# Kernel tuning notes

Measured on AMD Instinct MI355X. Metric: run time of the kernel, lower is better.

The kernel has to match this reference:

```python
import jax, jax.numpy as jnp
import numpy as np

N = 100000      # nodes
E = 1600000     # edges
D_IN = 100
D_OUT = 100


def _sage(x, src, dst, W_agg, W_root, b):
    """PyG SAGEConv, aggr='mean', root_weight=True:
    out = mean_{j in N(i)} x_j @ W_agg + x_i @ W_root + b
    Aggregation flows source -> target (dst gathers from src)."""
    num_nodes = x.shape[0]
    deg = jax.ops.segment_sum(jnp.ones((src.shape[0],), x.dtype), dst,
                              num_segments=num_nodes)
    agg = jax.ops.segment_sum(x[src], dst, num_segments=num_nodes)  # [N, D]
    agg = agg / jnp.maximum(deg, 1.0)[:, None]
    return agg @ W_agg + x @ W_root + b


def setup_inputs() -> dict:
    key = jax.random.key(0)
    ks = jax.random.split(key, 12)
    s = 0.05
    return {
        "x": jax.random.normal(ks[0], (N, D_IN), jnp.float32),
        "edge_index": jax.random.randint(ks[1], (2, E), 0, N, jnp.int32),
        "edge_weight": jax.random.uniform(ks[2], (E,), jnp.float32),
        "W_sage_agg": jax.random.normal(ks[3], (D_IN, D_OUT), jnp.float32) * s,
        "W_sage_root": jax.random.normal(ks[4], (D_IN, D_OUT), jnp.float32) * s,
        "b_sage": jnp.zeros((D_OUT,), jnp.float32),
        "W_mu_agg": jax.random.normal(ks[5], (D_OUT, D_OUT), jnp.float32) * s,
        "W_mu_root": jax.random.normal(ks[6], (D_OUT, D_OUT), jnp.float32) * s,
        "b_mu": jnp.zeros((D_OUT,), jnp.float32),
        "W_var_agg": jax.random.normal(ks[7], (D_OUT, D_OUT), jnp.float32) * s,
        "W_var_root": jax.random.normal(ks[8], (D_OUT, D_OUT), jnp.float32) * s,
        "b_var": jnp.zeros((D_OUT,), jnp.float32),
    }


def reference(x, edge_index, edge_weight,
              W_sage_agg, W_sage_root, b_sage,
              W_mu_agg, W_mu_root, b_mu,
              W_var_agg, W_var_root, b_var):
    # edge_weight is accepted but unused, matching the torch module.
    src, dst = edge_index[0], edge_index[1]
    feat = jax.nn.relu(_sage(x, src, dst, W_sage_agg, W_sage_root, b_sage))
    mu = _sage(feat, src, dst, W_mu_agg, W_mu_root, b_mu)
    var = _sage(feat, src, dst, W_var_agg, W_var_root, b_var)
    return (mu, var)
```

## Files before the change

### kernel.cpp

```cpp
#include <hip/hip_runtime.h>
#include <cstdint>
#include <cstddef>

#define N_NODES 100000
#define N_EDGES 1600000
#define DIM 100
#define DPAD 128
#define ROWS_ALLOC 100096

#define RPB 128
#define GEMM_GRID (ROWS_ALLOC / RPB)

#define KBUCK 500
#define NPB   200
#define BCAP  4096
#define EPB   6400

typedef __attribute__((ext_vector_type(8))) short s16x8;
typedef __attribute__((ext_vector_type(8))) unsigned short us8;
typedef __attribute__((ext_vector_type(4))) unsigned short us4;
typedef __attribute__((ext_vector_type(4))) float f32x4;
typedef __attribute__((ext_vector_type(2))) float f32x2;
typedef __attribute__((ext_vector_type(4))) unsigned int u32x4;

static __device__ __forceinline__ float bf2f(unsigned short h) {
    return __uint_as_float(((unsigned)h) << 16);
}
static __device__ __forceinline__ unsigned short f2bf(float f) {
    unsigned u = __float_as_uint(f);
    return (unsigned short)((u + 0x7FFFu + ((u >> 16) & 1u)) >> 16);
}

__global__ __launch_bounds__(256) void bucket_kernel(const int* __restrict__ ei,
                                                     unsigned* __restrict__ bucket_cur,
                                                     unsigned* __restrict__ regions) {
    __shared__ unsigned hist[KBUCK];
    __shared__ unsigned posl[KBUCK];
    int tid = threadIdx.x;
    int e0 = blockIdx.x * EPB;
    for (int i = tid; i < KBUCK; i += 256) hist[i] = 0;
    __syncthreads();
    for (int i = tid; i < EPB; i += 256) {
        int dst = ei[N_EDGES + e0 + i];
        int b = dst / NPB;
        atomicAdd(&hist[b], 1u);
    }
    __syncthreads();
    for (int i = tid; i < KBUCK; i += 256) {
        unsigned h = hist[i];
        posl[i] = h ? atomicAdd(&bucket_cur[i], h) : 0u;
    }
    __syncthreads();
    for (int i = tid; i < EPB; i += 256) {
        int src = ei[e0 + i];
        int dst = ei[N_EDGES + e0 + i];
        int b = dst / NPB;
        int dl = dst - b * NPB;
        unsigned r = atomicAdd(&posl[b], 1u);
        if (r < BCAP) regions[(size_t)b * BCAP + r] = ((unsigned)src << 8) | (unsigned)dl;
    }
}

__global__ __launch_bounds__(256) void csr_kernel(const unsigned* __restrict__ regions,
                                                  const unsigned* __restrict__ bucket_cur,
                                                  unsigned* __restrict__ gbase,
                                                  int* __restrict__ row_off,
                                                  int* __restrict__ cnt,
                                                  int* __restrict__ csr_src) {
    __shared__ unsigned hist[256];
    __shared__ unsigned sa[256], sb[256];
    __shared__ unsigned posl[256];
    __shared__ unsigned sh_gb;
    int tid = threadIdx.x;
    int b = blockIdx.x;
    unsigned total = bucket_cur[b];
    if (total > BCAP) total = BCAP;
    hist[tid] = 0;
    __syncthreads();
    const unsigned* reg = regions + (size_t)b * BCAP;
    for (unsigned e = tid; e < total; e += 256)
        atomicAdd(&hist[reg[e] & 0xFFu], 1u);
    __syncthreads();
    unsigned* cur = sa; unsigned* nxt = sb;
    cur[tid] = hist[tid];
    __syncthreads();
    for (int off = 1; off < 256; off <<= 1) {
        unsigned t = cur[tid];
        if (tid >= off) t += cur[tid - off];
        nxt[tid] = t;
        __syncthreads();
        unsigned* tmp = cur; cur = nxt; nxt = tmp;
    }
    unsigned excl = cur[tid] - hist[tid];
    if (tid == 0) sh_gb = atomicAdd(gbase, total);
    __syncthreads();
    unsigned gb = sh_gb;
    posl[tid] = gb + excl;
    if (tid < NPB) {
        int node = b * NPB + tid;
        cnt[node] = (int)hist[tid];
        row_off[node] = (int)(gb + excl);
    }
    __syncthreads();
    for (unsigned e = tid; e < total; e += 256) {
        unsigned p = reg[e];
        unsigned r = atomicAdd(&posl[p & 0xFFu], 1u);
        csr_src[r] = (int)(p >> 8);
    }
}

__global__ __launch_bounds__(256) void convert_pad(const float* __restrict__ X,
                                                   unsigned short* __restrict__ Xp) {
    int t = blockIdx.x * 256 + threadIdx.x;
    if (t >= N_NODES * 16) return;
    int node = t >> 4, chunk = t & 15;
    us8 o;
    if (chunk < 12) {
        const float4* p = (const float4*)(X + (size_t)node * DIM + chunk * 8);
        float4 a = p[0], b = p[1];
        o[0] = f2bf(a.x); o[1] = f2bf(a.y); o[2] = f2bf(a.z); o[3] = f2bf(a.w);
        o[4] = f2bf(b.x); o[5] = f2bf(b.y); o[6] = f2bf(b.z); o[7] = f2bf(b.w);
    } else if (chunk == 12) {
        const float4* p = (const float4*)(X + (size_t)node * DIM + 96);
        float4 a = p[0];
        o[0] = f2bf(a.x); o[1] = f2bf(a.y); o[2] = f2bf(a.z); o[3] = f2bf(a.w);
        o[4] = 0; o[5] = 0; o[6] = 0; o[7] = 0;
    } else {
        for (int i = 0; i < 8; ++i) o[i] = 0;
    }
    *(us8*)(Xp + (size_t)node * DPAD + chunk * 8) = o;
}

__global__ __launch_bounds__(256) void build_w(const float* __restrict__ W0, const float* __restrict__ W1,
                                               const float* __restrict__ W2, const float* __restrict__ W3,
                                               const float* __restrict__ W4, const float* __restrict__ W5,
                                               unsigned short* __restrict__ Wt) {
    int t = blockIdx.x * 256 + threadIdx.x;
    if (t >= 6 * DPAD * 16) return;
    int mat = t / (DPAD * 16);
    int rem = t % (DPAD * 16);
    int nrow = rem >> 4, chunk = rem & 15;
    const float* W = (mat == 0) ? W0 : (mat == 1) ? W1 : (mat == 2) ? W2
                   : (mat == 3) ? W3 : (mat == 4) ? W4 : W5;
    us8 o;
    #pragma unroll
    for (int j = 0; j < 8; ++j) {
        int k = chunk * 8 + j;
        float v = (k < DIM && nrow < DIM) ? W[(size_t)k * DIM + nrow] : 0.f;
        o[j] = f2bf(v);
    }
    *(us8*)(Wt + (size_t)mat * DPAD * DPAD + (size_t)nrow * DPAD + chunk * 8) = o;
}

__global__ __launch_bounds__(256) void build_bias(const float* __restrict__ b0, const float* __restrict__ b1,
                                                  const float* __restrict__ b2, float* __restrict__ bp) {
    int t = blockIdx.x * 256 + threadIdx.x;
    if (t >= 3 * DPAD) return;
    int mat = t / DPAD, i = t % DPAD;
    const float* b = (mat == 0) ? b0 : (mat == 1) ? b1 : b2;
    bp[t] = (i < DIM) ? b[i] : 0.f;
}

__global__ __launch_bounds__(256) void aggregate_pad(const unsigned short* __restrict__ Xh,
                                                     const int* __restrict__ csr_src,
                                                     const int* __restrict__ row_off,
                                                     const int* __restrict__ cnt,
                                                     unsigned short* __restrict__ outh, int n) {
    int node = blockIdx.x * 4 + (threadIdx.x >> 6);
    if (node >= n) return;
    int lane  = threadIdx.x & 63;
    int chunk = lane & 15;
    int slot  = lane >> 4;
    int start = row_off[node];
    int deg   = cnt[node];

    f32x2 acc2[4];
    #pragma unroll
    for (int k = 0; k < 4; ++k) acc2[k] = (f32x2){0.f, 0.f};

    const int coff = chunk * 8;
    int base = 0;
    for (; base + 16 <= deg; base += 16) {
        const int* ep = csr_src + start + base + slot * 4;
        int s0 = ep[0], s1 = ep[1], s2 = ep[2], s3 = ep[3];
        u32x4 w0 = *(const u32x4*)(Xh + (size_t)s0 * DPAD + coff);
        u32x4 w1 = *(const u32x4*)(Xh + (size_t)s1 * DPAD + coff);
        u32x4 w2 = *(const u32x4*)(Xh + (size_t)s2 * DPAD + coff);
        u32x4 w3 = *(const u32x4*)(Xh + (size_t)s3 * DPAD + coff);
        #pragma unroll
        for (int k = 0; k < 4; ++k) {
            acc2[k] += (f32x2){__uint_as_float(w0[k] << 16), __uint_as_float(w0[k] & 0xFFFF0000u)};
            acc2[k] += (f32x2){__uint_as_float(w1[k] << 16), __uint_as_float(w1[k] & 0xFFFF0000u)};
            acc2[k] += (f32x2){__uint_as_float(w2[k] << 16), __uint_as_float(w2[k] & 0xFFFF0000u)};
            acc2[k] += (f32x2){__uint_as_float(w3[k] << 16), __uint_as_float(w3[k] & 0xFFFF0000u)};
        }
    }
    if (base < deg) {
        int e0 = base + slot * 4;
        #pragma unroll
        for (int t = 0; t < 4; ++t) {
            int el = e0 + t;
            bool ok = el < deg;
            int eg = start + (ok ? el : (deg - 1));
            int s  = csr_src[eg];
            u32x4 w = *(const u32x4*)(Xh + (size_t)s * DPAD + coff);
            float mval = ok ? 1.f : 0.f;
            f32x2 mm = (f32x2){mval, mval};
            #pragma unroll
            for (int k = 0; k < 4; ++k) {
                f32x2 v = (f32x2){__uint_as_float(w[k] << 16), __uint_as_float(w[k] & 0xFFFF0000u)};
                acc2[k] += v * mm;
            }
        }
    }
    #pragma unroll
    for (int k = 0; k < 4; ++k) {
        acc2[k].x += __shfl_xor(acc2[k].x, 16, 64);
        acc2[k].y += __shfl_xor(acc2[k].y, 16, 64);
        acc2[k].x += __shfl_xor(acc2[k].x, 32, 64);
        acc2[k].y += __shfl_xor(acc2[k].y, 32, 64);
    }
    if (lane < 16) {
        float inv = 1.0f / (float)(deg > 0 ? deg : 1);
        us8 o;
        #pragma unroll
        for (int k = 0; k < 4; ++k) {
            o[2 * k]     = f2bf(acc2[k].x * inv);
            o[2 * k + 1] = f2bf(acc2[k].y * inv);
        }
        *(us8*)(outh + (size_t)node * DPAD + coff) = o;
    }
}

__global__ __launch_bounds__(256, 2) void gemm_l1_strip(const unsigned short* __restrict__ Aagg,
                                                        const unsigned short* __restrict__ Aroot,
                                                        const unsigned short* __restrict__ WtA,
                                                        const unsigned short* __restrict__ WtR,
                                                        const float* __restrict__ bpad,
                                                        unsigned short* __restrict__ outp) {
    int lane  = threadIdx.x & 63;
    int strip = threadIdx.x >> 6;
    int m16   = lane & 15;
    int quad  = lane >> 4;
    int row0  = blockIdx.x * RPB;

    s16x8 wf[2][2][4];
    const unsigned short* Ws[2] = {WtA, WtR};
    #pragma unroll
    for (int ph = 0; ph < 2; ++ph)
        #pragma unroll
        for (int nt = 0; nt < 2; ++nt)
            #pragma unroll
            for (int ks = 0; ks < 4; ++ks)
                wf[ph][nt][ks] = *(const s16x8*)(Ws[ph] + (size_t)(strip * 32 + nt * 16 + m16) * DPAD + ks * 32 + quad * 8);
    #pragma unroll
    for (int ph = 0; ph < 2; ++ph)
        #pragma unroll
        for (int nt = 0; nt < 2; ++nt)
            #pragma unroll
            for (int ks = 0; ks < 4; ++ks)
                asm volatile("" : "+v"(wf[ph][nt][ks]));

    float4 bias4[2];
    #pragma unroll
    for (int nt = 0; nt < 2; ++nt)
        bias4[nt] = *(const float4*)(bpad + strip * 32 + nt * 16 + quad * 4);

    s16x8 bA[2][4], bR[2][4];
    #pragma unroll
    for (int ks = 0; ks < 4; ++ks) {
        bA[0][ks] = *(const s16x8*)(Aagg  + (size_t)(row0 + m16) * DPAD + ks * 32 + quad * 8);
        bR[0][ks] = *(const s16x8*)(Aroot + (size_t)(row0 + m16) * DPAD + ks * 32 + quad * 8);
    }

    #pragma unroll
    for (int t = 0; t < RPB / 16; ++t) {
        int cur = t & 1;
        if (t < RPB / 16 - 1) {
            int mn = row0 + (t + 1) * 16 + m16;
            #pragma unroll
            for (int ks = 0; ks < 4; ++ks) {
                bA[cur ^ 1][ks] = *(const s16x8*)(Aagg  + (size_t)mn * DPAD + ks * 32 + quad * 8);
                bR[cur ^ 1][ks] = *(const s16x8*)(Aroot + (size_t)mn * DPAD + ks * 32 + quad * 8);
            }
        }
        f32x4 acc[2];
        acc[0] = (f32x4){0.f, 0.f, 0.f, 0.f};
        acc[1] = (f32x4){0.f, 0.f, 0.f, 0.f};
        #pragma unroll
        for (int ks = 0; ks < 4; ++ks) {
            acc[0] = __builtin_amdgcn_mfma_f32_16x16x32_bf16(wf[0][0][ks], bA[cur][ks], acc[0], 0, 0, 0);
            acc[1] = __builtin_amdgcn_mfma_f32_16x16x32_bf16(wf[0][1][ks], bA[cur][ks], acc[1], 0, 0, 0);
            acc[0] = __builtin_amdgcn_mfma_f32_16x16x32_bf16(wf[1][0][ks], bR[cur][ks], acc[0], 0, 0, 0);
            acc[1] = __builtin_amdgcn_mfma_f32_16x16x32_bf16(wf[1][1][ks], bR[cur][ks], acc[1], 0, 0, 0);
        }
        int m = row0 + t * 16 + m16;
        #pragma unroll
        for (int nt = 0; nt < 2; ++nt) {
            int col0 = strip * 32 + nt * 16 + quad * 4;
            us4 o;
            #pragma unroll
            for (int r = 0; r < 4; ++r) {
                float v = acc[nt][r] + ((const float*)&bias4[nt])[r];
                v = v > 0.f ? v : 0.f;
                o[r] = f2bf(v);
            }
            *(us4*)(outp + (size_t)m * DPAD + col0) = o;
        }
    }
}

__global__ __launch_bounds__(256, 2) void gemm_l2_strip(const unsigned short* __restrict__ Aagg,
                                                        const unsigned short* __restrict__ Afeat,
                                                        const unsigned short* __restrict__ WtMA,
                                                        const unsigned short* __restrict__ WtMR,
                                                        const unsigned short* __restrict__ WtVA,
                                                        const unsigned short* __restrict__ WtVR,
                                                        const float* __restrict__ bpm,
                                                        const float* __restrict__ bpv,
                                                        float* __restrict__ outMu,
                                                        float* __restrict__ outVar) {
    int lane  = threadIdx.x & 63;
    int strip = threadIdx.x >> 6;
    int m16   = lane & 15;
    int quad  = lane >> 4;
    int row0  = blockIdx.x * RPB;

    s16x8 wf[2][2][2][4];
    const unsigned short* Ws[2][2] = {{WtMA, WtMR}, {WtVA, WtVR}};
    #pragma unroll
    for (int hd = 0; hd < 2; ++hd)
        #pragma unroll
        for (int ph = 0; ph < 2; ++ph)
            #pragma unroll
            for (int nt = 0; nt < 2; ++nt)
                #pragma unroll
                for (int ks = 0; ks < 4; ++ks)
                    wf[hd][ph][nt][ks] = *(const s16x8*)(Ws[hd][ph] + (size_t)(strip * 32 + nt * 16 + m16) * DPAD + ks * 32 + quad * 8);
    #pragma unroll
    for (int hd = 0; hd < 2; ++hd)
        #pragma unroll
        for (int ph = 0; ph < 2; ++ph)
            #pragma unroll
            for (int nt = 0; nt < 2; ++nt)
                #pragma unroll
                for (int ks = 0; ks < 4; ++ks)
                    asm volatile("" : "+v"(wf[hd][ph][nt][ks]));

    float4 bm4[2], bv4[2];
    #pragma unroll
    for (int nt = 0; nt < 2; ++nt) {
        bm4[nt] = *(const float4*)(bpm + strip * 32 + nt * 16 + quad * 4);
        bv4[nt] = *(const float4*)(bpv + strip * 32 + nt * 16 + quad * 4);
    }

    s16x8 bA[2][4], bF[2][4];
    #pragma unroll
    for (int ks = 0; ks < 4; ++ks) {
        bA[0][ks] = *(const s16x8*)(Aagg  + (size_t)(row0 + m16) * DPAD + ks * 32 + quad * 8);
        bF[0][ks] = *(const s16x8*)(Afeat + (size_t)(row0 + m16) * DPAD + ks * 32 + quad * 8);
    }

    #pragma unroll
    for (int t = 0; t < RPB / 16; ++t) {
        int cur = t & 1;
        if (t < RPB / 16 - 1) {
            int mn = row0 + (t + 1) * 16 + m16;
            #pragma unroll
            for (int ks = 0; ks < 4; ++ks) {
                bA[cur ^ 1][ks] = *(const s16x8*)(Aagg  + (size_t)mn * DPAD + ks * 32 + quad * 8);
                bF[cur ^ 1][ks] = *(const s16x8*)(Afeat + (size_t)mn * DPAD + ks * 32 + quad * 8);
            }
        }
        f32x4 aM[2], aV[2];
        aM[0] = (f32x4){0.f,0.f,0.f,0.f}; aM[1] = (f32x4){0.f,0.f,0.f,0.f};
        aV[0] = (f32x4){0.f,0.f,0.f,0.f}; aV[1] = (f32x4){0.f,0.f,0.f,0.f};
        #pragma unroll
        for (int ks = 0; ks < 4; ++ks) {
            aM[0] = __builtin_amdgcn_mfma_f32_16x16x32_bf16(wf[0][0][0][ks], bA[cur][ks], aM[0], 0, 0, 0);
            aM[1] = __builtin_amdgcn_mfma_f32_16x16x32_bf16(wf[0][0][1][ks], bA[cur][ks], aM[1], 0, 0, 0);
            aV[0] = __builtin_amdgcn_mfma_f32_16x16x32_bf16(wf[1][0][0][ks], bA[cur][ks], aV[0], 0, 0, 0);
            aV[1] = __builtin_amdgcn_mfma_f32_16x16x32_bf16(wf[1][0][1][ks], bA[cur][ks], aV[1], 0, 0, 0);
            aM[0] = __builtin_amdgcn_mfma_f32_16x16x32_bf16(wf[0][1][0][ks], bF[cur][ks], aM[0], 0, 0, 0);
            aM[1] = __builtin_amdgcn_mfma_f32_16x16x32_bf16(wf[0][1][1][ks], bF[cur][ks], aM[1], 0, 0, 0);
            aV[0] = __builtin_amdgcn_mfma_f32_16x16x32_bf16(wf[1][1][0][ks], bF[cur][ks], aV[0], 0, 0, 0);
            aV[1] = __builtin_amdgcn_mfma_f32_16x16x32_bf16(wf[1][1][1][ks], bF[cur][ks], aV[1], 0, 0, 0);
        }
        int m = row0 + t * 16 + m16;
        if (m < N_NODES) {
            #pragma unroll
            for (int nt = 0; nt < 2; ++nt) {
                int col0 = strip * 32 + nt * 16 + quad * 4;
                if (col0 <= DIM - 4) {
                    float4 vm, vv;
                    vm.x = aM[nt][0] + bm4[nt].x; vm.y = aM[nt][1] + bm4[nt].y;
                    vm.z = aM[nt][2] + bm4[nt].z; vm.w = aM[nt][3] + bm4[nt].w;
                    vv.x = aV[nt][0] + bv4[nt].x; vv.y = aV[nt][1] + bv4[nt].y;
                    vv.z = aV[nt][2] + bv4[nt].z; vv.w = aV[nt][3] + bv4[nt].w;
                    *(float4*)(outMu  + (size_t)m * DIM + col0) = vm;
                    *(float4*)(outVar + (size_t)m * DIM + col0) = vv;
                }
            }
        }
    }
}

extern "C" void kernel_launch(void* const* d_in, const int* in_sizes, int n_in,
                              void* d_out, int out_size, void* d_ws, size_t ws_size,
                              hipStream_t stream) {
    const float* x   = (const float*)d_in[0];
    const int*   ei  = (const int*)d_in[1];
    const float* Wsa = (const float*)d_in[3];
    const float* Wsr = (const float*)d_in[4];
    const float* bs  = (const float*)d_in[5];
    const float* Wma = (const float*)d_in[6];
    const float* Wmr = (const float*)d_in[7];
    const float* bm  = (const float*)d_in[8];
    const float* Wva = (const float*)d_in[9];
    const float* Wvr = (const float*)d_in[10];
    const float* bv  = (const float*)d_in[11];

    float* out_mu  = (float*)d_out;
    float* out_var = out_mu + (size_t)N_NODES * DIM;

    char* ws = (char*)d_ws;
    int*      row_off    = (int*)(ws);
    int*      cnt        = (int*)(ws + 400000);
    unsigned* bucket_cur = (unsigned*)(ws + 800000);
    unsigned* gbase      = (unsigned*)(ws + 802048);
    int*      csr_src    = (int*)(ws + 802176);
    unsigned short* Wt   = (unsigned short*)(ws + 7202176);
    float*          bp   = (float*)(ws + 7398784);
    unsigned short* xp   = (unsigned short*)(ws + 7400448);
    unsigned short* aggp = (unsigned short*)(ws + 33025024);
    unsigned short* ftp  = (unsigned short*)(ws + 58649600);
    unsigned* regions    = (unsigned*)(ws + 7400448);

    unsigned short* WtSA = Wt;
    unsigned short* WtSR = Wt + 1 * DPAD * DPAD;
    unsigned short* WtMA = Wt + 2 * DPAD * DPAD;
    unsigned short* WtMR = Wt + 3 * DPAD * DPAD;
    unsigned short* WtVA = Wt + 4 * DPAD * DPAD;
    unsigned short* WtVR = Wt + 5 * DPAD * DPAD;
    float* bps = bp;
    float* bpm = bp + DPAD;
    float* bpv = bp + 2 * DPAD;

    hipMemsetAsync(bucket_cur, 0, 2048, stream);
    hipMemsetAsync(gbase, 0, 128, stream);

    bucket_kernel<<<N_EDGES / EPB, 256, 0, stream>>>(ei, bucket_cur, regions);
    csr_kernel<<<KBUCK, 256, 0, stream>>>(regions, bucket_cur, gbase, row_off, cnt, csr_src);

    convert_pad<<<(N_NODES * 16 + 255) / 256, 256, 0, stream>>>(x, xp);
    build_w<<<(6 * DPAD * 16 + 255) / 256, 256, 0, stream>>>(Wsa, Wsr, Wma, Wmr, Wva, Wvr, Wt);
    build_bias<<<2, 256, 0, stream>>>(bs, bm, bv, bp);

    aggregate_pad<<<N_NODES / 4, 256, 0, stream>>>(xp, csr_src, row_off, cnt, aggp, N_NODES);
    gemm_l1_strip<<<GEMM_GRID, 256, 0, stream>>>(aggp, xp, WtSA, WtSR, bps, ftp);

    aggregate_pad<<<N_NODES / 4, 256, 0, stream>>>(ftp, csr_src, row_off, cnt, aggp, N_NODES);
    gemm_l2_strip<<<GEMM_GRID, 256, 0, stream>>>(aggp, ftp, WtMA, WtMR, WtVA, WtVR,
                                                 bpm, bpv, out_mu, out_var);
}
```

Before: 403.2 us.

## Fuse edge bucketing and input conversion into one prep kernel, shrink buckets

Merges the edge bucketing, feature bf16 conversion, weight transpose and bias padding kernels into a single launch dispatched by block index, so the independent prep work runs concurrently. The bucket count doubles to 1000 with 100 nodes each and a 2048 capacity, and the regions buffer moves to the ftp area so it no longer overlaps xp, which is now written in the same kernel. The csr_kernel is launched with 1000 blocks, and its 256-entry histogram still covers 100 local nodes. The smaller capacity gives less headroom for skewed buckets, and edges past the cap are silently dropped.

Result: no change. 405.6 us (+0.6%).

```diff
diff --git a/kernel.cpp b/kernel.cpp
--- a/kernel.cpp
+++ b/kernel.cpp
@@ -11,10 +11,16 @@
 #define RPB 128
 #define GEMM_GRID (ROWS_ALLOC / RPB)
 
-#define KBUCK 500
-#define NPB   200
-#define BCAP  4096
+#define KBUCK 1000
+#define NPB   100
+#define BCAP  2048
 #define EPB   6400
+
+#define PREP_BUCKET_BLOCKS 250
+#define PREP_CONVERT_BLOCKS 6250
+#define PREP_BW_BLOCKS 48
+#define PREP_BIAS_BLOCKS 2
+#define PREP_GRID (PREP_BUCKET_BLOCKS + PREP_CONVERT_BLOCKS + PREP_BW_BLOCKS + PREP_BIAS_BLOCKS)
 
 typedef __attribute__((ext_vector_type(8))) short s16x8;
 typedef __attribute__((ext_vector_type(8))) unsigned short us8;
@@ -31,33 +37,86 @@
     return (unsigned short)((u + 0x7FFFu + ((u >> 16) & 1u)) >> 16);
 }
 
-__global__ __launch_bounds__(256) void bucket_kernel(const int* __restrict__ ei,
-                                                     unsigned* __restrict__ bucket_cur,
-                                                     unsigned* __restrict__ regions) {
+__global__ __launch_bounds__(256) void prep_fused(const int* __restrict__ ei,
+                                                  unsigned* __restrict__ bucket_cur,
+                                                  unsigned* __restrict__ regions,
+                                                  const float* __restrict__ X,
+                                                  unsigned short* __restrict__ Xp,
+                                                  const float* __restrict__ W0, const float* __restrict__ W1,
+                                                  const float* __restrict__ W2, const float* __restrict__ W3,
+                                                  const float* __restrict__ W4, const float* __restrict__ W5,
+                                                  unsigned short* __restrict__ Wt,
+                                                  const float* __restrict__ b0, const float* __restrict__ b1,
+                                                  const float* __restrict__ b2, float* __restrict__ bp) {
     __shared__ unsigned hist[KBUCK];
     __shared__ unsigned posl[KBUCK];
+    int bid = blockIdx.x;
     int tid = threadIdx.x;
-    int e0 = blockIdx.x * EPB;
-    for (int i = tid; i < KBUCK; i += 256) hist[i] = 0;
-    __syncthreads();
-    for (int i = tid; i < EPB; i += 256) {
-        int dst = ei[N_EDGES + e0 + i];
-        int b = dst / NPB;
-        atomicAdd(&hist[b], 1u);
-    }
-    __syncthreads();
-    for (int i = tid; i < KBUCK; i += 256) {
-        unsigned h = hist[i];
-        posl[i] = h ? atomicAdd(&bucket_cur[i], h) : 0u;
-    }
-    __syncthreads();
-    for (int i = tid; i < EPB; i += 256) {
-        int src = ei[e0 + i];
-        int dst = ei[N_EDGES + e0 + i];
-        int b = dst / NPB;
-        int dl = dst - b * NPB;
-        unsigned r = atomicAdd(&posl[b], 1u);
-        if (r < BCAP) regions[(size_t)b * BCAP + r] = ((unsigned)src << 8) | (unsigned)dl;
+
+    if (bid < PREP_BUCKET_BLOCKS) {
+        int e0 = bid * EPB;
+        for (int i = tid; i < KBUCK; i += 256) hist[i] = 0;
+        __syncthreads();
+        for (int i = tid; i < EPB; i += 256) {
+            int dst = ei[N_EDGES + e0 + i];
+            int b = dst / NPB;
+            atomicAdd(&hist[b], 1u);
+        }
+        __syncthreads();
+        for (int i = tid; i < KBUCK; i += 256) {
+            unsigned h = hist[i];
+            posl[i] = h ? atomicAdd(&bucket_cur[i], h) : 0u;
+        }
+        __syncthreads();
+        for (int i = tid; i < EPB; i += 256) {
+            int src = ei[e0 + i];
+            int dst = ei[N_EDGES + e0 + i];
+            int b = dst / NPB;
+            int dl = dst - b * NPB;
+            unsigned r = atomicAdd(&posl[b], 1u);
+            if (r < BCAP) regions[(size_t)b * BCAP + r] = ((unsigned)src << 8) | (unsigned)dl;
+        }
+    } else if (bid < PREP_BUCKET_BLOCKS + PREP_CONVERT_BLOCKS) {
+        int t = (bid - PREP_BUCKET_BLOCKS) * 256 + tid;
+        if (t >= N_NODES * 16) return;
+        int node = t >> 4, chunk = t & 15;
+        us8 o;
+        if (chunk < 12) {
+            const float4* p = (const float4*)(X + (size_t)node * DIM + chunk * 8);
+            float4 a = p[0], b = p[1];
+            o[0] = f2bf(a.x); o[1] = f2bf(a.y); o[2] = f2bf(a.z); o[3] = f2bf(a.w);
+            o[4] = f2bf(b.x); o[5] = f2bf(b.y); o[6] = f2bf(b.z); o[7] = f2bf(b.w);
+        } else if (chunk == 12) {
+            const float4* p = (const float4*)(X + (size_t)node * DIM + 96);
+            float4 a = p[0];
+            o[0] = f2bf(a.x); o[1] = f2bf(a.y); o[2] = f2bf(a.z); o[3] = f2bf(a.w);
+            o[4] = 0; o[5] = 0; o[6] = 0; o[7] = 0;
+        } else {
+            for (int i = 0; i < 8; ++i) o[i] = 0;
+        }
+        *(us8*)(Xp + (size_t)node * DPAD + chunk * 8) = o;
+    } else if (bid < PREP_BUCKET_BLOCKS + PREP_CONVERT_BLOCKS + PREP_BW_BLOCKS) {
+        int t = (bid - PREP_BUCKET_BLOCKS - PREP_CONVERT_BLOCKS) * 256 + tid;
+        if (t >= 6 * DPAD * 16) return;
+        int mat = t / (DPAD * 16);
+        int rem = t % (DPAD * 16);
+        int nrow = rem >> 4, chunk = rem & 15;
+        const float* W = (mat == 0) ? W0 : (mat == 1) ? W1 : (mat == 2) ? W2
+                       : (mat == 3) ? W3 : (mat == 4) ? W4 : W5;
+        us8 o;
+        #pragma unroll
+        for (int j = 0; j < 8; ++j) {
+            int k = chunk * 8 + j;
+            float v = (k < DIM && nrow < DIM) ? W[(size_t)k * DIM + nrow] : 0.f;
+            o[j] = f2bf(v);
+        }
+        *(us8*)(Wt + (size_t)mat * DPAD * DPAD + (size_t)nrow * DPAD + chunk * 8) = o;
+    } else {
+        int t = (bid - PREP_BUCKET_BLOCKS - PREP_CONVERT_BLOCKS - PREP_BW_BLOCKS) * 256 + tid;
+        if (t >= 3 * DPAD) return;
+        int mat = t / DPAD, i = t % DPAD;
+        const float* b = (mat == 0) ? b0 : (mat == 1) ? b1 : b2;
+        bp[t] = (i < DIM) ? b[i] : 0.f;
     }
 }
 
@@ -109,58 +168,6 @@
     }
 }
 
-__global__ __launch_bounds__(256) void convert_pad(const float* __restrict__ X,
-                                                   unsigned short* __restrict__ Xp) {
-    int t = blockIdx.x * 256 + threadIdx.x;
-    if (t >= N_NODES * 16) return;
-    int node = t >> 4, chunk = t & 15;
-    us8 o;
-    if (chunk < 12) {
-        const float4* p = (const float4*)(X + (size_t)node * DIM + chunk * 8);
-        float4 a = p[0], b = p[1];
-        o[0] = f2bf(a.x); o[1] = f2bf(a.y); o[2] = f2bf(a.z); o[3] = f2bf(a.w);
-        o[4] = f2bf(b.x); o[5] = f2bf(b.y); o[6] = f2bf(b.z); o[7] = f2bf(b.w);
-    } else if (chunk == 12) {
-        const float4* p = (const float4*)(X + (size_t)node * DIM + 96);
-        float4 a = p[0];
-        o[0] = f2bf(a.x); o[1] = f2bf(a.y); o[2] = f2bf(a.z); o[3] = f2bf(a.w);
-        o[4] = 0; o[5] = 0; o[6] = 0; o[7] = 0;
-    } else {
-        for (int i = 0; i < 8; ++i) o[i] = 0;
-    }
-    *(us8*)(Xp + (size_t)node * DPAD + chunk * 8) = o;
-}
-
-__global__ __launch_bounds__(256) void build_w(const float* __restrict__ W0, const float* __restrict__ W1,
-                                               const float* __restrict__ W2, const float* __restrict__ W3,
-                                               const float* __restrict__ W4, const float* __restrict__ W5,
-                                               unsigned short* __restrict__ Wt) {
-    int t = blockIdx.x * 256 + threadIdx.x;
-    if (t >= 6 * DPAD * 16) return;
-    int mat = t / (DPAD * 16);
-    int rem = t % (DPAD * 16);
-    int nrow = rem >> 4, chunk = rem & 15;
-    const float* W = (mat == 0) ? W0 : (mat == 1) ? W1 : (mat == 2) ? W2
-                   : (mat == 3) ? W3 : (mat == 4) ? W4 : W5;
-    us8 o;
-    #pragma unroll
-    for (int j = 0; j < 8; ++j) {
-        int k = chunk * 8 + j;
-        float v = (k < DIM && nrow < DIM) ? W[(size_t)k * DIM + nrow] : 0.f;
-        o[j] = f2bf(v);
-    }
-    *(us8*)(Wt + (size_t)mat * DPAD * DPAD + (size_t)nrow * DPAD + chunk * 8) = o;
-}
-
-__global__ __launch_bounds__(256) void build_bias(const float* __restrict__ b0, const float* __restrict__ b1,
-                                                  const float* __restrict__ b2, float* __restrict__ bp) {
-    int t = blockIdx.x * 256 + threadIdx.x;
-    if (t >= 3 * DPAD) return;
-    int mat = t / DPAD, i = t % DPAD;
-    const float* b = (mat == 0) ? b0 : (mat == 1) ? b1 : b2;
-    bp[t] = (i < DIM) ? b[i] : 0.f;
-}
-
 __global__ __launch_bounds__(256) void aggregate_pad(const unsigned short* __restrict__ Xh,
                                                      const int* __restrict__ csr_src,
                                                      const int* __restrict__ row_off,
@@ -427,14 +434,14 @@
     int*      row_off    = (int*)(ws);
     int*      cnt        = (int*)(ws + 400000);
     unsigned* bucket_cur = (unsigned*)(ws + 800000);
-    unsigned* gbase      = (unsigned*)(ws + 802048);
-    int*      csr_src    = (int*)(ws + 802176);
-    unsigned short* Wt   = (unsigned short*)(ws + 7202176);
-    float*          bp   = (float*)(ws + 7398784);
-    unsigned short* xp   = (unsigned short*)(ws + 7400448);
-    unsigned short* aggp = (unsigned short*)(ws + 33025024);
-    unsigned short* ftp  = (unsigned short*)(ws + 58649600);
-    unsigned* regions    = (unsigned*)(ws + 7400448);
+    unsigned* gbase      = (unsigned*)(ws + 804096);
+    int*      csr_src    = (int*)(ws + 804224);
+    unsigned short* Wt   = (unsigned short*)(ws + 7204224);
+    float*          bp   = (float*)(ws + 7400832);
+    unsigned short* xp   = (unsigned short*)(ws + 7402496);
+    unsigned short* aggp = (unsigned short*)(ws + 33027072);
+    unsigned short* ftp  = (unsigned short*)(ws + 58651648);
+    unsigned* regions    = (unsigned*)(ws + 58651648);
 
     unsigned short* WtSA = Wt;
     unsigned short* WtSR = Wt + 1 * DPAD * DPAD;
@@ -446,15 +453,13 @@
     float* bpm = bp + DPAD;
     float* bpv = bp + 2 * DPAD;
 
-    hipMemsetAsync(bucket_cur, 0, 2048, stream);
+    hipMemsetAsync(bucket_cur, 0, 4096, stream);
     hipMemsetAsync(gbase, 0, 128, stream);
 
-    bucket_kernel<<<N_EDGES / EPB, 256, 0, stream>>>(ei, bucket_cur, regions);
+    prep_fused<<<PREP_GRID, 256, 0, stream>>>(ei, bucket_cur, regions, x, xp,
+                                              Wsa, Wsr, Wma, Wmr, Wva, Wvr, Wt,
+                                              bs, bm, bv, bp);
     csr_kernel<<<KBUCK, 256, 0, stream>>>(regions, bucket_cur, gbase, row_off, cnt, csr_src);
-
-    convert_pad<<<(N_NODES * 16 + 255) / 256, 256, 0, stream>>>(x, xp);
-    build_w<<<(6 * DPAD * 16 + 255) / 256, 256, 0, stream>>>(Wsa, Wsr, Wma, Wmr, Wva, Wvr, Wt);
-    build_bias<<<2, 256, 0, stream>>>(bs, bm, bv, bp);
 
     aggregate_pad<<<N_NODES / 4, 256, 0, stream>>>(xp, csr_src, row_off, cnt, aggp, N_NODES);
     gemm_l1_strip<<<GEMM_GRID, 256, 0, stream>>>(aggp, xp, WtSA, WtSR, bps, ftp);
```
